# Performance work log

Measured on AMD Instinct MI355X. Metric: run time of the kernel, lower is better.

Reference implementation:

```python
import jax, jax.numpy as jnp
import numpy as np

NUM_HEADS = 16
KEY_DIM = 64
EPS = 1e-6


def setup_inputs() -> dict:
    key = jax.random.key(0)
    k0, k1, k2, k3, k4 = jax.random.split(key, 5)
    B, S, E = 4, 4096, NUM_HEADS * KEY_DIM
    scale = 1.0 / np.sqrt(KEY_DIM)
    return {
        "query": jax.random.normal(k0, (B, S, E), dtype=jnp.float32),
        "Wq": jax.random.normal(k1, (NUM_HEADS, KEY_DIM, KEY_DIM), dtype=jnp.float32) * scale,
        "Wk": jax.random.normal(k2, (NUM_HEADS, KEY_DIM, KEY_DIM), dtype=jnp.float32) * scale,
        "Wv": jax.random.normal(k3, (NUM_HEADS, KEY_DIM, KEY_DIM), dtype=jnp.float32) * scale,
        "Wo": jax.random.normal(k4, (E, E), dtype=jnp.float32) * (1.0 / np.sqrt(E)),
    }


def reference(query, Wq, Wk, Wv, Wo):
    # Self-attention: key = value = query (per call() defaults).
    B, S, E = query.shape
    H, D = NUM_HEADS, KEY_DIM
    # split_heads: (B, S, E) -> (B, H, S, D)
    x = jnp.transpose(query.reshape(B, S, H, D), (0, 2, 1, 3))
    # Per-head linear projections (all heads batched in one einsum each).
    q = jnp.einsum("bhsd,hde->bhse", x, Wq)
    k = jnp.einsum("bhsd,hde->bhse", x, Wk)
    v = jnp.einsum("bhsd,hde->bhse", x, Wv)
    # Kernel feature map phi(x) = elu(x) + 1 (strictly positive).
    phi_q = jax.nn.elu(q) + 1.0
    phi_k = jax.nn.elu(k) + 1.0
    # Linear (non-causal) attention: O(S*D^2) instead of O(S^2*D).
    kv = jnp.einsum("bhsd,bhse->bhde", phi_k, v)        # (B,H,D,D)
    k_sum = jnp.sum(phi_k, axis=2)                       # (B,H,D)
    z = jnp.einsum("bhsd,bhd->bhs", phi_q, k_sum)        # (B,H,S)
    ctx = jnp.einsum("bhsd,bhde->bhse", phi_q, kv) / (z[..., None] + EPS)
    # combine_heads: (B,H,S,D) -> (B,S,E), then output projection (no bias).
    combined = jnp.transpose(ctx, (0, 2, 1, 3)).reshape(B, S, H * D)
    return combined @ Wo
```

## Files before the change

kernel.cpp:

```cpp
#include <hip/hip_runtime.h>
#include <stdint.h>

#define S_LEN 4096
#define NHEADS 16
#define DHEAD 64
#define EMB 1024
#define NBATCH 4
#define NBH (NBATCH * NHEADS)

typedef unsigned short u16t;
typedef __attribute__((ext_vector_type(8))) short short8;
typedef __attribute__((ext_vector_type(4))) float f32x4;

__device__ __forceinline__ u16t f2bf(float f) {
  unsigned int x = __float_as_uint(f);
  x += 0x7fffu + ((x >> 16) & 1u);
  return (u16t)(x >> 16);
}
__device__ __forceinline__ unsigned int pack2(float a, float b) {
  return (unsigned int)f2bf(a) | ((unsigned int)f2bf(b) << 16);
}
__device__ __forceinline__ float bf2f(u16t u) { return __uint_as_float(((unsigned int)u) << 16); }
__device__ __forceinline__ float phifn(float v) { return v > 0.f ? v + 1.f : __expf(v); }

__device__ __forceinline__ void stage_w8k(const u16t* __restrict__ wg,
                                          u16t* __restrict__ lds, int t) {
#pragma unroll
  for (int c = 0; c < 2; ++c) {
    const u16t* src = wg + (size_t)(c * 256 + t) * 8;
    char* dst = (char*)lds + c * 4096 + ((t >> 6) << 10);
    __builtin_amdgcn_global_load_lds((const __attribute__((address_space(1))) unsigned int*)src,
                                     (__attribute__((address_space(3))) unsigned int*)dst,
                                     16, 0, 0);
  }
}

__global__ __launch_bounds__(256) void la_wprep(const float* __restrict__ Wq,
                                                const float* __restrict__ Wk,
                                                const float* __restrict__ Wv,
                                                const float* __restrict__ Wo,
                                                u16t* __restrict__ WqT,
                                                u16t* __restrict__ WkT,
                                                u16t* __restrict__ WvT,
                                                u16t* __restrict__ WoT) {
  __shared__ float tmp[64][65];
  int blk = blockIdx.x;
  int t = threadIdx.x;
  if (blk < 48) {
    int mat = blk >> 4, h = blk & 15;
    const float* src = (mat == 0 ? Wq : (mat == 1 ? Wk : Wv)) + (size_t)h * 4096;
    u16t* dst = (mat == 0 ? WqT : (mat == 1 ? WkT : WvT)) + (size_t)h * 4096;
#pragma unroll
    for (int p = 0; p < 16; ++p) {
      int i = p * 256 + t;
      tmp[i >> 6][i & 63] = src[i];
    }
    __syncthreads();
#pragma unroll
    for (int p = 0; p < 16; ++p) {
      int i = p * 256 + t;
      int e = i >> 6, r = i & 63, o = r >> 3, j = r & 7;
      dst[i] = f2bf(tmp[((o ^ (e & 7)) << 3) + j][e]);
    }
  } else {
    int bb = blk - 48;
    int n0 = (bb & 15) * 64, k0 = (bb >> 4) * 64;
    int tx = t & 63, ty = t >> 6;
    for (int r = ty; r < 64; r += 4) tmp[r][tx] = Wo[(size_t)(k0 + r) * EMB + n0 + tx];
    __syncthreads();
    for (int r = ty; r < 64; r += 4)
      WoT[(size_t)(n0 + r) * EMB + k0 + tx] = f2bf(tmp[tx][r]);
  }
}

__global__ __launch_bounds__(256) void la_kvq5(const float* __restrict__ q,
                                               const u16t* __restrict__ WqT,
                                               const u16t* __restrict__ WkT,
                                               const u16t* __restrict__ WvT,
                                               u16t* __restrict__ phiq,
                                               float* __restrict__ kvpart,
                                               float* __restrict__ kspart) {
  __shared__ u16t xs[64 * 72];
  __shared__ u16t wq[4096];
  __shared__ u16t wk[4096];
  __shared__ u16t wv[4096];
  __shared__ u16t pkT[64 * 72];
  __shared__ u16t vT[64 * 72];
  __shared__ float ksp4[4][64];
  int blk = blockIdx.x;
  int bh = blk >> 3, tile = blk & 7;
  int b = bh >> 4, h = bh & 15;
  int s0 = tile << 9;
  int t = threadIdx.x;
  int wave = t >> 6, lane = t & 63, l16 = lane & 15, g = lane >> 4;

  stage_w8k(WqT + (size_t)h * 4096, wq, t);
  stage_w8k(WkT + (size_t)h * 4096, wk, t);
  stage_w8k(WvT + (size_t)h * 4096, wv, t);

  const float* xg = q + ((size_t)b * S_LEN + s0) * EMB + h * 64;
  int pr_r = t >> 4, pr_c4 = (t & 15) * 4;

  float4 pre[4];
#pragma unroll
  for (int i = 0; i < 4; ++i)
    pre[i] = *(const float4*)(xg + (size_t)(i * 16 + pr_r) * EMB + pr_c4);

  f32x4 kacc[4];
#pragma unroll
  for (int n = 0; n < 4; ++n) kacc[n] = 0.f;
  float ks_acc = 0.f;
  int ks_e = t & 63, ks_q = t >> 6;

  for (int c = 0; c < 8; ++c) {
    if (c) __syncthreads();
#pragma unroll
    for (int i = 0; i < 4; ++i) {
      uint2 p;
      p.x = pack2(pre[i].x, pre[i].y);
      p.y = pack2(pre[i].z, pre[i].w);
      *(uint2*)(&xs[(i * 16 + pr_r) * 72 + pr_c4]) = p;
    }
    if (c < 7) {
#pragma unroll
      for (int i = 0; i < 4; ++i)
        pre[i] = *(const float4*)(xg + (size_t)((c + 1) * 64 + i * 16 + pr_r) * EMB + pr_c4);
    }
    __syncthreads();

    f32x4 aQ[4], aK[4], aV[4];
#pragma unroll
    for (int n = 0; n < 4; ++n) { aQ[n] = 0.f; aK[n] = 0.f; aV[n] = 0.f; }
    short8 af[2];
#pragma unroll
    for (int kk = 0; kk < 2; ++kk)
      af[kk] = *(const short8*)(&xs[(wave * 16 + l16) * 72 + kk * 32 + g * 8]);
#pragma unroll
    for (int n = 0; n < 4; ++n) {
      int e = n * 16 + l16;
#pragma unroll
      for (int kk = 0; kk < 2; ++kk) {
        int op = (kk * 4 + g) ^ (l16 & 7);
        short8 bQ = *(const short8*)(&wq[e * 64 + op * 8]);
        short8 bK = *(const short8*)(&wk[e * 64 + op * 8]);
        short8 bV = *(const short8*)(&wv[e * 64 + op * 8]);
        aQ[n] = __builtin_amdgcn_mfma_f32_16x16x32_bf16(af[kk], bQ, aQ[n], 0, 0, 0);
        aK[n] = __builtin_amdgcn_mfma_f32_16x16x32_bf16(af[kk], bK, aK[n], 0, 0, 0);
        aV[n] = __builtin_amdgcn_mfma_f32_16x16x32_bf16(af[kk], bV, aV[n], 0, 0, 0);
      }
    }
    __syncthreads();

#pragma unroll
    for (int n = 0; n < 4; ++n) {
      int e = n * 16 + l16;
      int sb = wave * 16 + g * 4;
      uint2 pk2, vv2;
      pk2.x = pack2(phifn(aK[n][0]), phifn(aK[n][1]));
      pk2.y = pack2(phifn(aK[n][2]), phifn(aK[n][3]));
      vv2.x = pack2(aV[n][0], aV[n][1]);
      vv2.y = pack2(aV[n][2], aV[n][3]);
      *(uint2*)(&pkT[e * 72 + sb]) = pk2;
      *(uint2*)(&vT[e * 72 + sb]) = vv2;
#pragma unroll
      for (int j = 0; j < 4; ++j) xs[(sb + j) * 72 + e] = f2bf(phifn(aQ[n][j]));
    }
    __syncthreads();

#pragma unroll
    for (int i = 0; i < 2; ++i) {
      int slot = i * 256 + t;
      int r = slot >> 3, cc = (slot & 7) * 8;
      *(uint4*)(phiq + ((size_t)bh * S_LEN + s0 + c * 64 + r) * 64 + cc) =
          *(const uint4*)(&xs[r * 72 + cc]);
    }
#pragma unroll
    for (int ks = 0; ks < 2; ++ks) {
      short8 pa = *(const short8*)(&pkT[(wave * 16 + l16) * 72 + ks * 32 + g * 8]);
#pragma unroll
      for (int n = 0; n < 4; ++n) {
        short8 vb = *(const short8*)(&vT[(n * 16 + l16) * 72 + ks * 32 + g * 8]);
        kacc[n] = __builtin_amdgcn_mfma_f32_16x16x32_bf16(pa, vb, kacc[n], 0, 0, 0);
      }
    }
#pragma unroll
    for (int i = 0; i < 4; ++i) {
      uint2 u = *(const uint2*)(&pkT[ks_e * 72 + ks_q * 16 + i * 4]);
      ks_acc += bf2f((u16t)(u.x & 0xffff)) + bf2f((u16t)(u.x >> 16)) +
                bf2f((u16t)(u.y & 0xffff)) + bf2f((u16t)(u.y >> 16));
    }
  }

  float* kp = kvpart + (size_t)blk * 4096;
#pragma unroll
  for (int n = 0; n < 4; ++n)
#pragma unroll
    for (int j = 0; j < 4; ++j)
      kp[(wave * 16 + g * 4 + j) * 64 + n * 16 + l16] = kacc[n][j];

  ksp4[ks_q][ks_e] = ks_acc;
  __syncthreads();
  if (t < 64)
    kspart[(size_t)blk * 64 + t] = ksp4[0][t] + ksp4[1][t] + ksp4[2][t] + ksp4[3][t];
}

__global__ __launch_bounds__(256) void la_red3(const float* __restrict__ kvpart,
                                               const float* __restrict__ kspart,
                                               const u16t* __restrict__ WoT,
                                               float* __restrict__ ksum_g,
                                               u16t* __restrict__ W2T) {
  __shared__ float kvs[64][65];
  __shared__ u16t aT[256 * 72];
  int bh = blockIdx.x;
  int b = bh >> 4, h = bh & 15;
  int t = threadIdx.x, wave = t >> 6, lane = t & 63, l16 = lane & 15, g = lane >> 4;

  float acc[16];
#pragma unroll
  for (int i = 0; i < 16; ++i) acc[i] = 0.f;
  for (int p = 0; p < 8; ++p) {
    const float* base = kvpart + ((size_t)bh * 8 + p) * 4096;
#pragma unroll
    for (int i = 0; i < 16; ++i) acc[i] += base[i * 256 + t];
  }
#pragma unroll
  for (int i = 0; i < 16; ++i) {
    int idx = i * 256 + t;
    kvs[idx >> 6][idx & 63] = acc[i];
  }
  if (t < 64) {
    float a = 0.f;
    for (int p = 0; p < 8; ++p) a += kspart[((size_t)bh * 8 + p) * 64 + t];
    ksum_g[(size_t)bh * 64 + t] = a;
  }
  __syncthreads();

  short8 kvbf[4][2];
#pragma unroll
  for (int n = 0; n < 4; ++n)
#pragma unroll
    for (int kk = 0; kk < 2; ++kk) {
      u16t* pp = (u16t*)&kvbf[n][kk];
#pragma unroll
      for (int i = 0; i < 8; ++i) pp[i] = f2bf(kvs[n * 16 + l16][kk * 32 + g * 8 + i]);
    }

  for (int ec = 0; ec < 4; ++ec) {
    if (ec) __syncthreads();
#pragma unroll
    for (int p = 0; p < 8; ++p) {
      int slot = p * 256 + t;
      int r = slot >> 3, cc = (slot & 7) * 8;
      *(uint4*)(&aT[r * 72 + cc]) =
          *(const uint4*)(WoT + (size_t)(ec * 256 + r) * 1024 + h * 64 + cc);
    }
    __syncthreads();
    f32x4 c2[4][4];
#pragma unroll
    for (int mi = 0; mi < 4; ++mi)
#pragma unroll
      for (int n = 0; n < 4; ++n) c2[mi][n] = 0.f;
#pragma unroll
    for (int kk = 0; kk < 2; ++kk)
#pragma unroll
      for (int mi = 0; mi < 4; ++mi) {
        short8 afr = *(const short8*)(&aT[(wave * 64 + mi * 16 + l16) * 72 + kk * 32 + g * 8]);
#pragma unroll
        for (int n = 0; n < 4; ++n)
          c2[mi][n] = __builtin_amdgcn_mfma_f32_16x16x32_bf16(afr, kvbf[n][kk], c2[mi][n], 0, 0, 0);
      }
    __syncthreads();
#pragma unroll
    for (int mi = 0; mi < 4; ++mi)
#pragma unroll
      for (int n = 0; n < 4; ++n)
#pragma unroll
        for (int j = 0; j < 4; ++j)
          aT[(wave * 64 + mi * 16 + g * 4 + j) * 72 + n * 16 + l16] = f2bf(c2[mi][n][j]);
    __syncthreads();
#pragma unroll
    for (int p = 0; p < 8; ++p) {
      int slot = p * 256 + t;
      int r = slot >> 3, cc = (slot & 7) * 8;
      *(uint4*)(W2T + ((size_t)b << 20) + (size_t)(ec * 256 + r) * 1024 + h * 64 + cc) =
          *(const uint4*)(&aT[r * 72 + cc]);
    }
  }
}

__global__ __launch_bounds__(256) void la_scale(const u16t* __restrict__ phiq,
                                                const float* __restrict__ ksum_g,
                                                u16t* __restrict__ phiq2) {
  __shared__ float ks[64];
  int blk = blockIdx.x;
  int bh = blk >> 4, sl = blk & 15;
  int b = bh >> 4, h = bh & 15;
  int s0 = sl * 256;
  int t = threadIdx.x;
  if (t < 64) ks[t] = ksum_g[(size_t)bh * 64 + t];
  __syncthreads();
  int c16 = t & 15, rg = t >> 4;
#pragma unroll 2
  for (int it = 0; it < 16; ++it) {
    int s = s0 + it * 16 + rg;
    uint2 u = *(const uint2*)(phiq + ((size_t)bh * S_LEN + s) * 64 + c16 * 4);
    float f0 = bf2f((u16t)(u.x & 0xffff)), f1 = bf2f((u16t)(u.x >> 16));
    float f2 = bf2f((u16t)(u.y & 0xffff)), f3 = bf2f((u16t)(u.y >> 16));
    float zp = f0 * ks[c16 * 4] + f1 * ks[c16 * 4 + 1] + f2 * ks[c16 * 4 + 2] + f3 * ks[c16 * 4 + 3];
    zp += __shfl_xor(zp, 1);
    zp += __shfl_xor(zp, 2);
    zp += __shfl_xor(zp, 4);
    zp += __shfl_xor(zp, 8);
    float inv = 1.f / (zp + 1e-6f);
    uint2 o;
    o.x = pack2(f0 * inv, f1 * inv);
    o.y = pack2(f2 * inv, f3 * inv);
    *(uint2*)(phiq2 + ((size_t)(b * S_LEN + s)) * EMB + h * 64 + c16 * 4) = o;
  }
}

__device__ __forceinline__ void stage_half(const u16t* __restrict__ gbase,
                                           u16t* __restrict__ lbuf,
                                           int half, int t) {
#pragma unroll
  for (int it = 0; it < 2; ++it) {
    int slot = it * 512 + t;
    int row = half * 128 + (slot >> 3);
    int oct = slot & 7;
    const u16t* src = gbase + (size_t)row * EMB + (((oct ^ (row & 7)) << 3));
    char* dst = (char*)lbuf + ((half * 128 + it * 64 + ((t >> 6) << 3)) << 7);
    __builtin_amdgcn_global_load_lds((const __attribute__((address_space(1))) unsigned int*)src,
                                     (__attribute__((address_space(3))) unsigned int*)dst,
                                     16, 0, 0);
  }
}

#define GFENCE asm volatile("" ::: "memory")

#define LOAD_A(QM)                                                              \
  _Pragma("unroll") for (int mi = 0; mi < 4; ++mi) _Pragma("unroll")            \
      for (int kk = 0; kk < 2; ++kk) {                                          \
    int rr = (QM) * 128 + wr2 * 64 + mi * 16 + l16;                             \
    afr[mi][kk] = *(const short8*)((const char*)Acur + rr * 128 +               \
                                   ((((kk << 2) | g) ^ (rr & 7)) << 4));        \
  }
#define LOAD_B(QN, DST)                                                         \
  _Pragma("unroll") for (int ni = 0; ni < 2; ++ni) _Pragma("unroll")            \
      for (int kk = 0; kk < 2; ++kk) {                                          \
    int rr = (QN) * 128 + wc2 * 32 + ni * 16 + l16;                             \
    DST[ni][kk] = *(const short8*)((const char*)Bcur + rr * 128 +               \
                                   ((((kk << 2) | g) ^ (rr & 7)) << 4));        \
  }
#define MFMA_Q(QM, QN, BF)                                                      \
  __builtin_amdgcn_s_setprio(1);                                                \
  _Pragma("unroll") for (int mi = 0; mi < 4; ++mi) _Pragma("unroll")            \
      for (int ni = 0; ni < 2; ++ni) {                                          \
    acc[QM][QN][mi][ni] = __builtin_amdgcn_mfma_f32_16x16x32_bf16(              \
        afr[mi][0], BF[ni][0], acc[QM][QN][mi][ni], 0, 0, 0);                   \
    acc[QM][QN][mi][ni] = __builtin_amdgcn_mfma_f32_16x16x32_bf16(              \
        afr[mi][1], BF[ni][1], acc[QM][QN][mi][ni], 0, 0, 0);                   \
  }                                                                             \
  __builtin_amdgcn_s_setprio(0);

#define BAR()                      \
  __builtin_amdgcn_s_barrier();    \
  GFENCE

__global__ __launch_bounds__(512, 2) void la_gemm9(const u16t* __restrict__ A,
                                                   const u16t* __restrict__ W2T,
                                                   float* __restrict__ C) {
  __shared__ u16t Al[2][16384];
  __shared__ u16t Bl[2][16384];
  int t = threadIdx.x;
  int bid = blockIdx.x;
  int swz = ((bid & 7) << 5) + (bid >> 3);
  int mt = swz >> 2, nt = swz & 3;
  const int M0 = mt * 256, N0 = nt * 256;
  const int b = mt >> 4;
  int wave = t >> 6, lane = t & 63;
  int l16 = lane & 15, g = lane >> 4;
  int wr2 = wave >> 2, wc2 = wave & 3;

  f32x4 acc[2][2][4][2];
#pragma unroll
  for (int qm = 0; qm < 2; ++qm)
#pragma unroll
    for (int qn = 0; qn < 2; ++qn)
#pragma unroll
      for (int mi = 0; mi < 4; ++mi)
#pragma unroll
        for (int ni = 0; ni < 2; ++ni) acc[qm][qn][mi][ni] = 0.f;

  const u16t* Asrc = A + (size_t)M0 * EMB;
  const u16t* Bsrc = W2T + ((size_t)b << 20) + (size_t)N0 * EMB;

  stage_half(Asrc, Al[0], 0, t);
  stage_half(Bsrc, Bl[0], 0, t);
  stage_half(Bsrc, Bl[0], 1, t);
  stage_half(Asrc, Al[0], 1, t);
  asm volatile("s_waitcnt vmcnt(4)" ::: "memory");
  BAR();

  short8 afr[4][2], bf0[2][2], bf1[2][2];

  for (int kt = 0; kt < 15; ++kt) {
    const u16t* Acur = Al[kt & 1];
    const u16t* Bcur = Bl[kt & 1];
    u16t* Anxt = Al[(kt + 1) & 1];
    u16t* Bnxt = Bl[(kt + 1) & 1];
    const u16t* An = Asrc + (kt + 1) * 64;
    const u16t* Bn = Bsrc + (kt + 1) * 64;
    LOAD_A(0);
    LOAD_B(0, bf0);
    stage_half(An, Anxt, 0, t);
    stage_half(Bn, Bnxt, 0, t);
    asm volatile("s_waitcnt vmcnt(6)" ::: "memory");
    BAR();
    MFMA_Q(0, 0, bf0);
    GFENCE;
    BAR();
    LOAD_B(1, bf1);
    stage_half(Bn, Bnxt, 1, t);
    asm volatile("s_waitcnt vmcnt(6)" ::: "memory");
    BAR();
    MFMA_Q(0, 1, bf1);
    GFENCE;
    BAR();
    LOAD_A(1);
    stage_half(An, Anxt, 1, t);
    BAR();
    MFMA_Q(1, 1, bf1);
    GFENCE;
    BAR();
    asm volatile("s_waitcnt vmcnt(4)" ::: "memory");
    BAR();
    MFMA_Q(1, 0, bf0);
    GFENCE;
    BAR();
  }
  {
    const u16t* Acur = Al[1];
    const u16t* Bcur = Bl[1];
    LOAD_A(0);
    LOAD_B(0, bf0);
    asm volatile("s_waitcnt vmcnt(2)" ::: "memory");
    BAR();
    MFMA_Q(0, 0, bf0);
    GFENCE;
    BAR();
    LOAD_B(1, bf1);
    asm volatile("s_waitcnt vmcnt(0)" ::: "memory");
    BAR();
    MFMA_Q(0, 1, bf1);
    GFENCE;
    BAR();
    LOAD_A(1);
    BAR();
    MFMA_Q(1, 1, bf1);
    GFENCE;
    BAR();
    BAR();
    MFMA_Q(1, 0, bf0);
    GFENCE;
  }

#pragma unroll
  for (int qm = 0; qm < 2; ++qm)
#pragma unroll
    for (int qn = 0; qn < 2; ++qn)
#pragma unroll
      for (int mi = 0; mi < 4; ++mi)
#pragma unroll
        for (int ni = 0; ni < 2; ++ni)
#pragma unroll
          for (int j = 0; j < 4; ++j) {
            int row = M0 + qm * 128 + wr2 * 64 + mi * 16 + g * 4 + j;
            int col = N0 + qn * 128 + wc2 * 32 + ni * 16 + l16;
            C[(size_t)row * EMB + col] = acc[qm][qn][mi][ni][j];
          }
}

extern "C" void kernel_launch(void* const* d_in, const int* in_sizes, int n_in,
                              void* d_out, int out_size, void* d_ws, size_t ws_size,
                              hipStream_t stream) {
  const float* query = (const float*)d_in[0];
  const float* Wq = (const float*)d_in[1];
  const float* Wk = (const float*)d_in[2];
  const float* Wv = (const float*)d_in[3];
  const float* Wo = (const float*)d_in[4];
  float* out = (float*)d_out;
  char* ws = (char*)d_ws;

  u16t* WoT     = (u16t*)(ws);
  u16t* WqT     = (u16t*)(ws + 2097152);
  u16t* WkT     = (u16t*)(ws + 2228224);
  u16t* WvT     = (u16t*)(ws + 2359296);
  u16t* phiq    = (u16t*)(ws + 2490368);
  float* kvpart = (float*)(ws + 36044800);
  float* kspart = (float*)(ws + 44433408);
  float* ksum_g = (float*)(ws + 44564480);
  u16t* W2T     = (u16t*)(ws + 44580864);
  u16t* phiq2   = (u16t*)(ws + 52969472);

  la_wprep<<<304, 256, 0, stream>>>(Wq, Wk, Wv, Wo, WqT, WkT, WvT, WoT);
  la_kvq5<<<512, 256, 0, stream>>>(query, WqT, WkT, WvT, phiq, kvpart, kspart);
  la_red3<<<NBH, 256, 0, stream>>>(kvpart, kspart, WoT, ksum_g, W2T);
  la_scale<<<1024, 256, 0, stream>>>(phiq, ksum_g, phiq2);
  la_gemm9<<<256, 512, 0, stream>>>(phiq2, W2T, out);
}
```

Measured before the change: 106.5 us.

## Fold 1/z normalization into output GEMM and read phiq in head-major layout

The scale kernel no longer writes a rescaled, head-interleaved copy of phi_q. A small kernel now computes only the per-row 1/z values, and the final GEMM reads phi_q directly in its (b,h,s,d) layout. In the GEMM, each 64-wide K tile is one head, so each K-step's MFMA result goes into a temporary and is scaled by that row's 1/z before being added to the accumulator. This removes an 8 MB bf16 write and read pass, but adds extra FMAs, temporary accumulator registers and shared-memory reads of 1/z inside the GEMM inner loop, which may raise register pressure.

```diff
diff --git a/kernel.cpp b/kernel.cpp
--- a/kernel.cpp
+++ b/kernel.cpp
@@ -288,35 +288,45 @@
   }
 }
 
-__global__ __launch_bounds__(256) void la_scale(const u16t* __restrict__ phiq,
-                                                const float* __restrict__ ksum_g,
-                                                u16t* __restrict__ phiq2) {
-  __shared__ float ks[64];
+__global__ __launch_bounds__(256) void la_z(const u16t* __restrict__ phiq,
+                                            const float* __restrict__ ksum_g,
+                                            float* __restrict__ invz_g) {
+  __shared__ float ksl[16 * 64];
+  __shared__ float zbuf[64][17];
   int blk = blockIdx.x;
-  int bh = blk >> 4, sl = blk & 15;
-  int b = bh >> 4, h = bh & 15;
-  int s0 = sl * 256;
+  int b = blk >> 6, s0 = (blk & 63) * 64;
   int t = threadIdx.x;
-  if (t < 64) ks[t] = ksum_g[(size_t)bh * 64 + t];
+  int h = t >> 4, sl = t & 15;
+  *(float4*)(&ksl[t * 4]) = *(const float4*)(ksum_g + (size_t)b * 1024 + t * 4);
   __syncthreads();
-  int c16 = t & 15, rg = t >> 4;
-#pragma unroll 2
-  for (int it = 0; it < 16; ++it) {
-    int s = s0 + it * 16 + rg;
-    uint2 u = *(const uint2*)(phiq + ((size_t)bh * S_LEN + s) * 64 + c16 * 4);
-    float f0 = bf2f((u16t)(u.x & 0xffff)), f1 = bf2f((u16t)(u.x >> 16));
-    float f2 = bf2f((u16t)(u.y & 0xffff)), f3 = bf2f((u16t)(u.y >> 16));
-    float zp = f0 * ks[c16 * 4] + f1 * ks[c16 * 4 + 1] + f2 * ks[c16 * 4 + 2] + f3 * ks[c16 * 4 + 3];
-    zp += __shfl_xor(zp, 1);
-    zp += __shfl_xor(zp, 2);
-    zp += __shfl_xor(zp, 4);
-    zp += __shfl_xor(zp, 8);
-    float inv = 1.f / (zp + 1e-6f);
-    uint2 o;
-    o.x = pack2(f0 * inv, f1 * inv);
-    o.y = pack2(f2 * inv, f3 * inv);
-    *(uint2*)(phiq2 + ((size_t)(b * S_LEN + s)) * EMB + h * 64 + c16 * 4) = o;
-  }
+#pragma unroll
+  for (int j = 0; j < 4; ++j) {
+    int s = s0 + j * 16 + sl;
+    const uint4* pr = (const uint4*)(phiq + ((size_t)(b * 16 + h) * S_LEN + s) * 64);
+    float z = 0.f;
+#pragma unroll
+    for (int u = 0; u < 8; ++u) {
+      uint4 w = pr[u];
+      const float* kd = &ksl[h * 64 + u * 8];
+      z = fmaf(bf2f((u16t)(w.x & 0xffff)), kd[0], z);
+      z = fmaf(bf2f((u16t)(w.x >> 16)), kd[1], z);
+      z = fmaf(bf2f((u16t)(w.y & 0xffff)), kd[2], z);
+      z = fmaf(bf2f((u16t)(w.y >> 16)), kd[3], z);
+      z = fmaf(bf2f((u16t)(w.z & 0xffff)), kd[4], z);
+      z = fmaf(bf2f((u16t)(w.z >> 16)), kd[5], z);
+      z = fmaf(bf2f((u16t)(w.w & 0xffff)), kd[6], z);
+      z = fmaf(bf2f((u16t)(w.w >> 16)), kd[7], z);
+    }
+    zbuf[j * 16 + sl][h] = 1.f / (z + 1e-6f);
+  }
+  __syncthreads();
+  int h2 = t >> 4, c = (t & 15) * 4;
+  float4 o;
+  o.x = zbuf[c][h2];
+  o.y = zbuf[c + 1][h2];
+  o.z = zbuf[c + 2][h2];
+  o.w = zbuf[c + 3][h2];
+  *(float4*)(invz_g + (size_t)(b * 16 + h2) * S_LEN + s0 + c) = o;
 }
 
 __device__ __forceinline__ void stage_half(const u16t* __restrict__ gbase,
@@ -334,6 +344,21 @@
                                      16, 0, 0);
   }
 }
+__device__ __forceinline__ void stage_half_A(const u16t* __restrict__ gbase,
+                                             u16t* __restrict__ lbuf,
+                                             int half, int t) {
+#pragma unroll
+  for (int it = 0; it < 2; ++it) {
+    int slot = it * 512 + t;
+    int row = half * 128 + (slot >> 3);
+    int oct = slot & 7;
+    const u16t* src = gbase + (size_t)row * 64 + (((oct ^ (row & 7)) << 3));
+    char* dst = (char*)lbuf + ((half * 128 + it * 64 + ((t >> 6) << 3)) << 7);
+    __builtin_amdgcn_global_load_lds((const __attribute__((address_space(1))) unsigned int*)src,
+                                     (__attribute__((address_space(3))) unsigned int*)dst,
+                                     16, 0, 0);
+  }
+}
 
 #define GFENCE asm volatile("" ::: "memory")
 
@@ -351,32 +376,46 @@
     DST[ni][kk] = *(const short8*)((const char*)Bcur + rr * 128 +               \
                                    ((((kk << 2) | g) ^ (rr & 7)) << 4));        \
   }
-#define MFMA_Q(QM, QN, BF)                                                      \
-  __builtin_amdgcn_s_setprio(1);                                                \
-  _Pragma("unroll") for (int mi = 0; mi < 4; ++mi) _Pragma("unroll")            \
-      for (int ni = 0; ni < 2; ++ni) {                                          \
-    acc[QM][QN][mi][ni] = __builtin_amdgcn_mfma_f32_16x16x32_bf16(              \
-        afr[mi][0], BF[ni][0], acc[QM][QN][mi][ni], 0, 0, 0);                   \
-    acc[QM][QN][mi][ni] = __builtin_amdgcn_mfma_f32_16x16x32_bf16(              \
-        afr[mi][1], BF[ni][1], acc[QM][QN][mi][ni], 0, 0, 0);                   \
-  }                                                                             \
-  __builtin_amdgcn_s_setprio(0);
+#define MFMA_QS(QM, QN, BF, KT)                                                 \
+  {                                                                             \
+    f32x4 tq[4][2];                                                             \
+    _Pragma("unroll") for (int mi = 0; mi < 4; ++mi) _Pragma("unroll")          \
+        for (int ni = 0; ni < 2; ++ni) tq[mi][ni] = 0.f;                        \
+    __builtin_amdgcn_s_setprio(1);                                              \
+    _Pragma("unroll") for (int mi = 0; mi < 4; ++mi) _Pragma("unroll")          \
+        for (int ni = 0; ni < 2; ++ni) {                                        \
+      tq[mi][ni] = __builtin_amdgcn_mfma_f32_16x16x32_bf16(                     \
+          afr[mi][0], BF[ni][0], tq[mi][ni], 0, 0, 0);                          \
+      tq[mi][ni] = __builtin_amdgcn_mfma_f32_16x16x32_bf16(                     \
+          afr[mi][1], BF[ni][1], tq[mi][ni], 0, 0, 0);                          \
+    }                                                                           \
+    __builtin_amdgcn_s_setprio(0);                                              \
+    _Pragma("unroll") for (int mi = 0; mi < 4; ++mi)                            \
+      _Pragma("unroll") for (int j = 0; j < 4; ++j) {                           \
+        float zz = invzt[(KT) * 256 + (QM) * 128 + wr2 * 64 + mi * 16 + g * 4 + j]; \
+        _Pragma("unroll") for (int ni = 0; ni < 2; ++ni)                        \
+          acc[QM][QN][mi][ni][j] = fmaf(zz, tq[mi][ni][j], acc[QM][QN][mi][ni][j]); \
+      }                                                                         \
+  }
 
 #define BAR()                      \
   __builtin_amdgcn_s_barrier();    \
   GFENCE
 
-__global__ __launch_bounds__(512, 2) void la_gemm9(const u16t* __restrict__ A,
-                                                   const u16t* __restrict__ W2T,
-                                                   float* __restrict__ C) {
+__global__ __launch_bounds__(512, 2) void la_gemm13(const u16t* __restrict__ phiq,
+                                                    const u16t* __restrict__ W2T,
+                                                    const float* __restrict__ invz_g,
+                                                    float* __restrict__ C) {
   __shared__ u16t Al[2][16384];
   __shared__ u16t Bl[2][16384];
+  __shared__ float invzt[16 * 256];
   int t = threadIdx.x;
   int bid = blockIdx.x;
   int swz = ((bid & 7) << 5) + (bid >> 3);
   int mt = swz >> 2, nt = swz & 3;
   const int M0 = mt * 256, N0 = nt * 256;
   const int b = mt >> 4;
+  const int moff = M0 & 4095;
   int wave = t >> 6, lane = t & 63;
   int l16 = lane & 15, g = lane >> 4;
   int wr2 = wave >> 2, wc2 = wave & 3;
@@ -391,14 +430,21 @@
 #pragma unroll
         for (int ni = 0; ni < 2; ++ni) acc[qm][qn][mi][ni] = 0.f;
 
-  const u16t* Asrc = A + (size_t)M0 * EMB;
   const u16t* Bsrc = W2T + ((size_t)b << 20) + (size_t)N0 * EMB;
-
-  stage_half(Asrc, Al[0], 0, t);
+#define ASRC(KT) (phiq + ((size_t)(b * 16 + (KT)) * S_LEN + moff) * 64)
+
+  const float* zsrc = invz_g + (size_t)(b * 16) * S_LEN + moff;
+  int zk = t >> 5, zr = (t & 31) * 8;
+  float4 zv0 = *(const float4*)(zsrc + (size_t)zk * S_LEN + zr);
+  float4 zv1 = *(const float4*)(zsrc + (size_t)zk * S_LEN + zr + 4);
+  stage_half_A(ASRC(0), Al[0], 0, t);
   stage_half(Bsrc, Bl[0], 0, t);
   stage_half(Bsrc, Bl[0], 1, t);
-  stage_half(Asrc, Al[0], 1, t);
-  asm volatile("s_waitcnt vmcnt(4)" ::: "memory");
+  stage_half_A(ASRC(0), Al[0], 1, t);
+  asm volatile("s_waitcnt vmcnt(8)" ::: "memory");
+  *(float4*)(&invzt[zk * 256 + zr]) = zv0;
+  *(float4*)(&invzt[zk * 256 + zr + 4]) = zv1;
+  asm volatile("s_waitcnt vmcnt(4) lgkmcnt(0)" ::: "memory");
   BAR();
 
   short8 afr[4][2], bf0[2][2], bf1[2][2];
@@ -408,33 +454,33 @@
     const u16t* Bcur = Bl[kt & 1];
     u16t* Anxt = Al[(kt + 1) & 1];
     u16t* Bnxt = Bl[(kt + 1) & 1];
-    const u16t* An = Asrc + (kt + 1) * 64;
+    const u16t* An = ASRC(kt + 1);
     const u16t* Bn = Bsrc + (kt + 1) * 64;
     LOAD_A(0);
     LOAD_B(0, bf0);
-    stage_half(An, Anxt, 0, t);
+    stage_half_A(An, Anxt, 0, t);
     stage_half(Bn, Bnxt, 0, t);
     asm volatile("s_waitcnt vmcnt(6)" ::: "memory");
     BAR();
-    MFMA_Q(0, 0, bf0);
+    MFMA_QS(0, 0, bf0, kt);
     GFENCE;
     BAR();
     LOAD_B(1, bf1);
     stage_half(Bn, Bnxt, 1, t);
     asm volatile("s_waitcnt vmcnt(6)" ::: "memory");
     BAR();
-    MFMA_Q(0, 1, bf1);
+    MFMA_QS(0, 1, bf1, kt);
     GFENCE;
     BAR();
     LOAD_A(1);
-    stage_half(An, Anxt, 1, t);
-    BAR();
-    MFMA_Q(1, 1, bf1);
+    stage_half_A(An, Anxt, 1, t);
+    BAR();
+    MFMA_QS(1, 1, bf1, kt);
     GFENCE;
     BAR();
     asm volatile("s_waitcnt vmcnt(4)" ::: "memory");
     BAR();
-    MFMA_Q(1, 0, bf0);
+    MFMA_QS(1, 0, bf0, kt);
     GFENCE;
     BAR();
   }
@@ -445,22 +491,22 @@
     LOAD_B(0, bf0);
     asm volatile("s_waitcnt vmcnt(2)" ::: "memory");
     BAR();
-    MFMA_Q(0, 0, bf0);
+    MFMA_QS(0, 0, bf0, 15);
     GFENCE;
     BAR();
     LOAD_B(1, bf1);
     asm volatile("s_waitcnt vmcnt(0)" ::: "memory");
     BAR();
-    MFMA_Q(0, 1, bf1);
+    MFMA_QS(0, 1, bf1, 15);
     GFENCE;
     BAR();
     LOAD_A(1);
     BAR();
-    MFMA_Q(1, 1, bf1);
-    GFENCE;
-    BAR();
-    BAR();
-    MFMA_Q(1, 0, bf0);
+    MFMA_QS(1, 1, bf1, 15);
+    GFENCE;
+    BAR();
+    BAR();
+    MFMA_QS(1, 0, bf0, 15);
     GFENCE;
   }
 
@@ -478,6 +524,7 @@
             int col = N0 + qn * 128 + wc2 * 32 + ni * 16 + l16;
             C[(size_t)row * EMB + col] = acc[qm][qn][mi][ni][j];
           }
+#undef ASRC
 }
 
 extern "C" void kernel_launch(void* const* d_in, const int* in_sizes, int n_in,
@@ -500,11 +547,11 @@
   float* kspart = (float*)(ws + 44433408);
   float* ksum_g = (float*)(ws + 44564480);
   u16t* W2T     = (u16t*)(ws + 44580864);
-  u16t* phiq2   = (u16t*)(ws + 52969472);
+  float* invz   = (float*)(ws + 52969472);
 
   la_wprep<<<304, 256, 0, stream>>>(Wq, Wk, Wv, Wo, WqT, WkT, WvT, WoT);
   la_kvq5<<<512, 256, 0, stream>>>(query, WqT, WkT, WvT, phiq, kvpart, kspart);
   la_red3<<<NBH, 256, 0, stream>>>(kvpart, kspart, WoT, ksum_g, W2T);
-  la_scale<<<1024, 256, 0, stream>>>(phiq, ksum_g, phiq2);
-  la_gemm9<<<256, 512, 0, stream>>>(phiq2, W2T, out);
-}
+  la_z<<<256, 256, 0, stream>>>(phiq, ksum_g, invz);
+  la_gemm13<<<256, 512, 0, stream>>>(phiq, W2T, invz, out);
+}
```

New measurement: 112.1 us. 5.3% more time.
